# Performance work log

Hardware: AMD Instinct MI355X
Metric: run time of the kernel (lower is better)

Reference implementation:

```python
import jax, jax.numpy as jnp
import numpy as np
from jax import lax

# Module dims (match init_kwargs / input_specs)
CIN, COUT, K, STRIDE = 8, 16, 3, 2
U = V = 32                      # input spatial size (inshape = (CIN, U, V))
UO = VO = U // STRIDE           # 'same' padding with stride -> 16
IN_DIM = CIN * U * V + 1        # 8193 (homogeneous)
OUT_DIM = COUT * UO * VO + 1    # 4097 (homogeneous)
N = 1024                        # batch (columns of x_affine)


def setup_inputs() -> dict:
    key = jax.random.key(0)
    k1, k2, k3, k4, k5 = jax.random.split(key, 5)
    w = jax.random.normal(k1, (COUT, CIN, K, K), dtype=jnp.float32) * 0.1
    b = jax.random.normal(k2, (COUT,), dtype=jnp.float32) * 0.1
    # Keying matrices (dense stand-ins for the sparse keys); scaled to keep values sane.
    A = jax.random.normal(k3, (OUT_DIM, OUT_DIM), dtype=jnp.float32) / np.sqrt(OUT_DIM)
    Ainv = jax.random.normal(k4, (IN_DIM, IN_DIM), dtype=jnp.float32) / np.sqrt(IN_DIM)
    x_affine = jax.random.normal(k5, (IN_DIM, N), dtype=jnp.float32)
    return {"w": w, "b": b, "A": A, "Ainv": Ainv, "x_affine": x_affine}


def _toeplitz_conv_apply(z, w, b):
    """Apply the affine Toeplitz conv matrix T to z of shape (CIN*U*V+1, N).
    T = [[conv, bias], [0, 1]] so T@z = [conv(z[:-1]) + b*z[-1]; z[-1]]."""
    n = z.shape[1]
    hom = z[-1]                                   # (N,) homogeneous row
    x = z[:-1].T.reshape(n, CIN, U, V)            # (N, CIN, U, V)
    y = lax.conv_general_dilated(
        x, w, window_strides=(STRIDE, STRIDE), padding="SAME",
        dimension_numbers=("NCHW", "OIHW", "NCHW"))  # (N, COUT, UO, VO)
    y = y + b[None, :, None, None] * hom[:, None, None, None]
    yf = y.reshape(n, COUT * UO * VO).T           # (COUT*UO*VO, N)
    return jnp.concatenate([yf, hom[None, :]], axis=0)  # (OUT_DIM, N)


def reference(w, b, A, Ainv, x_affine):
    # What @ x = A @ T @ Ainv @ x  (factored; never materializes What)
    z = Ainv @ x_affine                # (IN_DIM, N)
    t = _toeplitz_conv_apply(z, w, b)  # (OUT_DIM, N)
    return A @ t                       # (OUT_DIM, N)
```

## Files before the change

kernel.cpp:

```cpp
#include <hip/hip_runtime.h>

#define IN_DIM 8193
#define OUT_DIM 4097
#define NB 1024
#define MP1 8320
#define KP1 8256
#define MP2 4224
#define KP2 4160

typedef __attribute__((ext_vector_type(8))) short short8;
typedef __attribute__((ext_vector_type(4))) float f32x4;

__device__ __forceinline__ unsigned short f2bf(float f) {
  unsigned int u = __float_as_uint(f);
  u = (u + 0x7fffu + ((u >> 16) & 1u)) >> 16;
  return (unsigned short)u;
}

__global__ __launch_bounds__(256) void cvt_pad_kernel(
    const float* __restrict__ src, unsigned short* __restrict__ dst,
    int sR, int sC, int dR, int dC) {
  int gid = blockIdx.x * 256 + threadIdx.x;
  int i4 = gid * 4;
  if (i4 >= dR * dC) return;
  int r = i4 / dC;
  int c = i4 - r * dC;
  unsigned short o[4];
#pragma unroll
  for (int j = 0; j < 4; ++j) {
    int cc = c + j;
    float v = (r < sR && cc < sC) ? src[(size_t)r * sC + cc] : 0.f;
    o[j] = f2bf(v);
  }
  unsigned int lo = (unsigned)o[0] | ((unsigned)o[1] << 16);
  unsigned int hi = (unsigned)o[2] | ((unsigned)o[3] << 16);
  *reinterpret_cast<uint2*>(dst + i4) = make_uint2(lo, hi);
}

__global__ __launch_bounds__(256) void transpose_cvt_kernel(
    const float* __restrict__ src, unsigned short* __restrict__ dst,
    int K, int N, int Kp) {
  __shared__ float tl[32][33];
  const int ntk = Kp >> 5;
  int bx = blockIdx.x % ntk;
  int by = blockIdx.x / ntk;
  int k0 = bx * 32, n0 = by * 32;
  int tx = threadIdx.x & 31, ty = threadIdx.x >> 5;
#pragma unroll
  for (int i = 0; i < 4; ++i) {
    int k = k0 + ty + i * 8;
    tl[ty + i * 8][tx] = (k < K) ? src[(size_t)k * N + n0 + tx] : 0.f;
  }
  __syncthreads();
#pragma unroll
  for (int i = 0; i < 4; ++i) {
    int n = n0 + ty + i * 8;
    dst[(size_t)n * Kp + k0 + tx] = f2bf(tl[tx][ty + i * 8]);
  }
}

__global__ __launch_bounds__(512, 4) void gemm_bt(
    const unsigned short* __restrict__ Ab,
    const unsigned short* __restrict__ Bt,
    float* __restrict__ C,
    int Kp, int Mout, int N) {
  __shared__ unsigned short As[128 * 64];
  __shared__ unsigned short Bs[128 * 64];
  const int tid = threadIdx.x;
  const int wid = tid >> 6;
  const int lane = tid & 63;
  const int nbm = gridDim.x >> 3;
  const int full = (nbm & ~7) << 3;
  int bm, bn;
  {
    const int i = blockIdx.x;
    if (i < full) {
      bm = ((i >> 6) << 3) + (i & 7);
      bn = (i >> 3) & 7;
    } else {
      const int r = i - full;
      bm = (full >> 3) + (r >> 3);
      bn = r & 7;
    }
  }
  const int m0 = bm << 7, n0 = bn << 7;
  const int wm = (wid >> 2) << 6;
  const int wn = (wid & 3) << 5;

  f32x4 acc[4][2] = {};

  const int nk = Kp >> 6;
  for (int kt = 0; kt < nk; ++kt) {
    const int k0 = kt << 6;
#pragma unroll
    for (int i = 0; i < 2; ++i) {
      const int s = i * 512 + tid;
      const int row = s >> 3;
      const int gl = (s & 7) ^ (row & 7);
      const unsigned short* ga = Ab + (size_t)(m0 + row) * Kp + (k0 + gl * 8);
      const unsigned short* gb = Bt + (size_t)(n0 + row) * Kp + (k0 + gl * 8);
      unsigned short* la = As + (size_t)(i * 512 + wid * 64) * 8;
      unsigned short* lb = Bs + (size_t)(i * 512 + wid * 64) * 8;
      __builtin_amdgcn_global_load_lds(
          (const __attribute__((address_space(1))) void*)ga,
          (__attribute__((address_space(3))) void*)la, 16, 0, 0);
      __builtin_amdgcn_global_load_lds(
          (const __attribute__((address_space(1))) void*)gb,
          (__attribute__((address_space(3))) void*)lb, 16, 0, 0);
    }
    __syncthreads();
#pragma unroll
    for (int kk = 0; kk < 2; ++kk) {
      short8 af[4], bfr[2];
#pragma unroll
      for (int mf = 0; mf < 4; ++mf) {
        const int row = wm + mf * 16 + (lane & 15);
        const int g = (kk * 4 + (lane >> 4)) ^ (row & 7);
        af[mf] = *reinterpret_cast<const short8*>(As + row * 64 + g * 8);
      }
#pragma unroll
      for (int nf = 0; nf < 2; ++nf) {
        const int row = wn + nf * 16 + (lane & 15);
        const int g = (kk * 4 + (lane >> 4)) ^ (row & 7);
        bfr[nf] = *reinterpret_cast<const short8*>(Bs + row * 64 + g * 8);
      }
#pragma unroll
      for (int mf = 0; mf < 4; ++mf)
#pragma unroll
        for (int nf = 0; nf < 2; ++nf)
          asm volatile("v_mfma_f32_16x16x32_bf16 %0, %1, %2, %0"
                       : "+v"(acc[mf][nf])
                       : "v"(af[mf]), "v"(bfr[nf]));
    }
    __syncthreads();
  }
#pragma unroll
  for (int mf = 0; mf < 4; ++mf) {
    const int rbase = m0 + wm + mf * 16 + (lane >> 4) * 4;
#pragma unroll
    for (int nf = 0; nf < 2; ++nf) {
      const int col = n0 + wn + nf * 16 + (lane & 15);
#pragma unroll
      for (int r = 0; r < 4; ++r) {
        const int row = rbase + r;
        if (row < Mout) C[(size_t)row * N + col] = acc[mf][nf][r];
      }
    }
  }
}

__global__ __launch_bounds__(256) void conv_tT_kernel(
    const float* __restrict__ z, const float* __restrict__ w,
    const float* __restrict__ bias, unsigned short* __restrict__ tT) {
  const int gid = blockIdx.x * 256 + threadIdx.x;
  const int n = gid & 1023;
  const int rg = gid >> 10;
  const int r0 = rg << 3;
  const float hom = z[(size_t)8192 * 1024 + n];
  unsigned short o[8];
  if (r0 >= 4096) {
#pragma unroll
    for (int j = 0; j < 8; ++j) o[j] = f2bf((r0 + j == 4096) ? hom : 0.f);
  } else {
    const int co = r0 >> 8;
    const int uo = (r0 >> 4) & 15;
    const int vo0 = r0 & 15;
    float acc[8];
    const float bb = bias[co];
#pragma unroll
    for (int j = 0; j < 8; ++j) acc[j] = bb * hom;
    for (int ci = 0; ci < 8; ++ci) {
#pragma unroll
      for (int kh = 0; kh < 3; ++kh) {
        const int u = uo * 2 + kh;
        if (u >= 32) continue;
        const float* zbase = z + (size_t)(ci * 1024 + u * 32) * 1024 + n;
#pragma unroll
        for (int kw = 0; kw < 3; ++kw) {
          const float wv = w[((co * 8 + ci) * 3 + kh) * 3 + kw];
#pragma unroll
          for (int j = 0; j < 8; ++j) {
            const int v = (vo0 + j) * 2 + kw;
            if (v < 32) acc[j] += wv * zbase[(size_t)v * 1024];
          }
        }
      }
    }
#pragma unroll
    for (int j = 0; j < 8; ++j) o[j] = f2bf(acc[j]);
  }
  uint4 pv;
  pv.x = (unsigned)o[0] | ((unsigned)o[1] << 16);
  pv.y = (unsigned)o[2] | ((unsigned)o[3] << 16);
  pv.z = (unsigned)o[4] | ((unsigned)o[5] << 16);
  pv.w = (unsigned)o[6] | ((unsigned)o[7] << 16);
  *reinterpret_cast<uint4*>(tT + (size_t)n * KP2 + r0) = pv;
}

extern "C" void kernel_launch(void* const* d_in, const int* in_sizes, int n_in,
                              void* d_out, int out_size, void* d_ws, size_t ws_size,
                              hipStream_t stream) {
  const float* w    = (const float*)d_in[0];
  const float* bias = (const float*)d_in[1];
  const float* A    = (const float*)d_in[2];
  const float* Ainv = (const float*)d_in[3];
  const float* x    = (const float*)d_in[4];
  float* out = (float*)d_out;

  char* ws = (char*)d_ws;
  size_t off = 0;
  unsigned short* Ainv_b = (unsigned short*)(ws + off); off += (size_t)MP1 * KP1 * 2;
  unsigned short* xT_b   = (unsigned short*)(ws + off); off += (size_t)NB * KP1 * 2;
  float*          z      = (float*)(ws + off);          off += (size_t)IN_DIM * NB * 4;
  unsigned short* A2_b   = (unsigned short*)(ws + off); off += (size_t)MP2 * KP2 * 2;
  unsigned short* tT_b   = (unsigned short*)(ws + off); off += (size_t)NB * KP2 * 2;
  (void)ws_size; (void)in_sizes; (void)n_in; (void)out_size;

  cvt_pad_kernel<<<(MP1 * KP1 / 4 + 255) / 256, 256, 0, stream>>>(
      Ainv, Ainv_b, IN_DIM, IN_DIM, MP1, KP1);
  transpose_cvt_kernel<<<(KP1 / 32) * (NB / 32), 256, 0, stream>>>(
      x, xT_b, IN_DIM, NB, KP1);
  cvt_pad_kernel<<<(MP2 * KP2 / 4 + 255) / 256, 256, 0, stream>>>(
      A, A2_b, OUT_DIM, OUT_DIM, MP2, KP2);
  gemm_bt<<<(MP1 / 128) * (NB / 128), 512, 0, stream>>>(
      Ainv_b, xT_b, z, KP1, IN_DIM, NB);
  conv_tT_kernel<<<(520 * 1024) / 256, 256, 0, stream>>>(z, w, bias, tT_b);
  gemm_bt<<<(MP2 / 128) * (NB / 128), 512, 0, stream>>>(
      A2_b, tT_b, out, KP2, OUT_DIM, NB);
}
```

Before: 440.5 us.

## Split-K both GEMMs with partial buffers reduced in conv and a sum kernel

Adds a split-K mode to the bf16 MFMA GEMM. The first GEMM (65x8 tiles) now runs as 2 K-splits, and the conv kernel sums the two partial z buffers as it reads them. The second GEMM (33x8 = 264 tiles, too few for 256 CUs at several blocks per CU) runs as 4 K-splits, and a new float4 reduction kernel writes the final output. Workspace buffers are aliased, with A2 reusing z2's space and the output partials reusing Ainv_b's space, so conversion of A is moved after the conv. The goal is to fill the GPU better, at the cost of extra partial-sum traffic and one more launch.

```diff
diff --git a/kernel.cpp b/kernel.cpp
--- a/kernel.cpp
+++ b/kernel.cpp
@@ -63,34 +63,41 @@
     const unsigned short* __restrict__ Ab,
     const unsigned short* __restrict__ Bt,
     float* __restrict__ C,
-    int Kp, int Mout, int N) {
+    int Kp, int Mout, int N, int Mp, int nsplit) {
   __shared__ unsigned short As[128 * 64];
   __shared__ unsigned short Bs[128 * 64];
   const int tid = threadIdx.x;
   const int wid = tid >> 6;
   const int lane = tid & 63;
-  const int nbm = gridDim.x >> 3;
+  const int nbm = Mp >> 7;
+  const int nbn = N >> 7;
+  const int bps = nbm * nbn;
+  const int sp = blockIdx.x / bps;
+  const int j = blockIdx.x - sp * bps;
   const int full = (nbm & ~7) << 3;
   int bm, bn;
-  {
-    const int i = blockIdx.x;
-    if (i < full) {
-      bm = ((i >> 6) << 3) + (i & 7);
-      bn = (i >> 3) & 7;
-    } else {
-      const int r = i - full;
-      bm = (full >> 3) + (r >> 3);
-      bn = r & 7;
-    }
+  if (j < full) {
+    bm = ((j >> 6) << 3) + (j & 7);
+    bn = (j >> 3) & 7;
+  } else {
+    const int r = j - full;
+    bm = (full >> 3) + (r >> 3);
+    bn = r & 7;
   }
   const int m0 = bm << 7, n0 = bn << 7;
   const int wm = (wid >> 2) << 6;
   const int wn = (wid & 3) << 5;
 
+  const int nk = Kp >> 6;
+  const int q = nk / nsplit, rr = nk - q * nsplit;
+  const int kt0 = sp * q + (sp < rr ? sp : rr);
+  const int ktn = q + (sp < rr ? 1 : 0);
+
+  float* Cp = C + (size_t)sp * Mout * N;
+
   f32x4 acc[4][2] = {};
 
-  const int nk = Kp >> 6;
-  for (int kt = 0; kt < nk; ++kt) {
+  for (int kt = kt0; kt < kt0 + ktn; ++kt) {
     const int k0 = kt << 6;
 #pragma unroll
     for (int i = 0; i < 2; ++i) {
@@ -143,20 +150,22 @@
 #pragma unroll
       for (int r = 0; r < 4; ++r) {
         const int row = rbase + r;
-        if (row < Mout) C[(size_t)row * N + col] = acc[mf][nf][r];
+        if (row < Mout) Cp[(size_t)row * N + col] = acc[mf][nf][r];
       }
     }
   }
 }
 
 __global__ __launch_bounds__(256) void conv_tT_kernel(
-    const float* __restrict__ z, const float* __restrict__ w,
-    const float* __restrict__ bias, unsigned short* __restrict__ tT) {
+    const float* __restrict__ za, const float* __restrict__ zb,
+    const float* __restrict__ w, const float* __restrict__ bias,
+    unsigned short* __restrict__ tT) {
   const int gid = blockIdx.x * 256 + threadIdx.x;
   const int n = gid & 1023;
   const int rg = gid >> 10;
   const int r0 = rg << 3;
-  const float hom = z[(size_t)8192 * 1024 + n];
+  const size_t homoff = (size_t)8192 * 1024 + n;
+  const float hom = za[homoff] + zb[homoff];
   unsigned short o[8];
   if (r0 >= 4096) {
 #pragma unroll
@@ -174,14 +183,17 @@
       for (int kh = 0; kh < 3; ++kh) {
         const int u = uo * 2 + kh;
         if (u >= 32) continue;
-        const float* zbase = z + (size_t)(ci * 1024 + u * 32) * 1024 + n;
+        const size_t zoff = (size_t)(ci * 1024 + u * 32) * 1024 + n;
 #pragma unroll
         for (int kw = 0; kw < 3; ++kw) {
           const float wv = w[((co * 8 + ci) * 3 + kh) * 3 + kw];
 #pragma unroll
           for (int j = 0; j < 8; ++j) {
             const int v = (vo0 + j) * 2 + kw;
-            if (v < 32) acc[j] += wv * zbase[(size_t)v * 1024];
+            if (v < 32) {
+              const size_t e = zoff + (size_t)v * 1024;
+              acc[j] += wv * (za[e] + zb[e]);
+            }
           }
         }
       }
@@ -195,6 +207,24 @@
   pv.z = (unsigned)o[4] | ((unsigned)o[5] << 16);
   pv.w = (unsigned)o[6] | ((unsigned)o[7] << 16);
   *reinterpret_cast<uint4*>(tT + (size_t)n * KP2 + r0) = pv;
+}
+
+__global__ __launch_bounds__(256) void sum4_kernel(
+    const float* __restrict__ p, float* __restrict__ out, int n4) {
+  const int i = blockIdx.x * 256 + threadIdx.x;
+  if (i >= n4) return;
+  const size_t stride4 = (size_t)OUT_DIM * NB / 4;
+  const float4* p4 = (const float4*)p;
+  float4 a = p4[i];
+  float4 b = p4[i + stride4];
+  float4 c = p4[i + 2 * stride4];
+  float4 d = p4[i + 3 * stride4];
+  float4 r;
+  r.x = (a.x + b.x) + (c.x + d.x);
+  r.y = (a.y + b.y) + (c.y + d.y);
+  r.z = (a.z + b.z) + (c.z + d.z);
+  r.w = (a.w + b.w) + (c.w + d.w);
+  reinterpret_cast<float4*>(out)[i] = r;
 }
 
 extern "C" void kernel_launch(void* const* d_in, const int* in_sizes, int n_in,
@@ -208,23 +238,27 @@
   float* out = (float*)d_out;
 
   char* ws = (char*)d_ws;
-  size_t off = 0;
-  unsigned short* Ainv_b = (unsigned short*)(ws + off); off += (size_t)MP1 * KP1 * 2;
-  unsigned short* xT_b   = (unsigned short*)(ws + off); off += (size_t)NB * KP1 * 2;
-  float*          z      = (float*)(ws + off);          off += (size_t)IN_DIM * NB * 4;
-  unsigned short* A2_b   = (unsigned short*)(ws + off); off += (size_t)MP2 * KP2 * 2;
-  unsigned short* tT_b   = (unsigned short*)(ws + off); off += (size_t)NB * KP2 * 2;
+  unsigned short* Ainv_b = (unsigned short*)(ws);
+  unsigned short* xT_b   = (unsigned short*)(ws + (size_t)MP1 * KP1 * 2);
+  float*          z2     = (float*)(ws + (size_t)MP1 * KP1 * 2 + (size_t)NB * KP1 * 2);
+  unsigned short* tT_b   = (unsigned short*)(ws + (size_t)MP1 * KP1 * 2 + (size_t)NB * KP1 * 2
+                                             + (size_t)2 * IN_DIM * NB * 4);
+  unsigned short* A2_b   = (unsigned short*)z2;
+  float*          outp   = (float*)Ainv_b;
   (void)ws_size; (void)in_sizes; (void)n_in; (void)out_size;
 
   cvt_pad_kernel<<<(MP1 * KP1 / 4 + 255) / 256, 256, 0, stream>>>(
       Ainv, Ainv_b, IN_DIM, IN_DIM, MP1, KP1);
   transpose_cvt_kernel<<<(KP1 / 32) * (NB / 32), 256, 0, stream>>>(
       x, xT_b, IN_DIM, NB, KP1);
+  gemm_bt<<<2 * (MP1 / 128) * (NB / 128), 512, 0, stream>>>(
+      Ainv_b, xT_b, z2, KP1, IN_DIM, NB, MP1, 2);
+  conv_tT_kernel<<<(520 * 1024) / 256, 256, 0, stream>>>(
+      z2, z2 + (size_t)IN_DIM * NB, w, bias, tT_b);
   cvt_pad_kernel<<<(MP2 * KP2 / 4 + 255) / 256, 256, 0, stream>>>(
       A, A2_b, OUT_DIM, OUT_DIM, MP2, KP2);
-  gemm_bt<<<(MP1 / 128) * (NB / 128), 512, 0, stream>>>(
-      Ainv_b, xT_b, z, KP1, IN_DIM, NB);
-  conv_tT_kernel<<<(520 * 1024) / 256, 256, 0, stream>>>(z, w, bias, tT_b);
-  gemm_bt<<<(MP2 / 128) * (NB / 128), 512, 0, stream>>>(
-      A2_b, tT_b, out, KP2, OUT_DIM, NB);
-}
+  gemm_bt<<<4 * (MP2 / 128) * (NB / 128), 512, 0, stream>>>(
+      A2_b, tT_b, outp, KP2, OUT_DIM, NB, MP2, 4);
+  const int n4 = OUT_DIM * NB / 4;
+  sum4_kernel<<<(n4 + 255) / 256, 256, 0, stream>>>(outp, out, n4);
+}
```

Measured after the change: 528.5 us. +20.0%, slower.
